# Kernel optimization log

Measured on AMD Instinct MI355X. Metric: run time of the kernel, lower is better.

## Reference

```python
import jax, jax.numpy as jnp
import numpy as np

CLIP = 1e5  # state-update clip bound from the original code

def _H(x):
    # smooth heaviside: (tanh(1e7*x)+1)/2
    return (jnp.tanh(1e7 * x) + 1.0) * 0.5

def _interception(Prec, PET, INSC):
    insc = jnp.clip(INSC * 5.0, 0.5, 5.0)
    IMAX = jnp.maximum(jnp.minimum(insc, PET), 0.0)
    INT = jnp.maximum(jnp.minimum(IMAX, Prec), 0.0)
    INR = jnp.maximum(Prec - INT, 0.0)
    return INT, INR

def _sms_store(SMS1, SMSC):
    S = jnp.clip(SMSC * 500.0, 50.0, 500.0)
    return jnp.maximum(jnp.minimum(SMS1, S), 0.0)

def _soil_fluxes(PET, INT, INR, COEFF, SQ, SMSC, SUB, CRAK, SMS1):
    C = jnp.clip(COEFF * 400.0, 50.0, 400.0)
    q = jnp.clip(SQ * 6.0, 0.0, 6.0)
    S = jnp.clip(SMSC * 500.0, 50.0, 500.0)
    sub = jnp.clip(SUB, 0.0, 1.0)
    crak = jnp.clip(CRAK, 0.0, 1.0)
    infil = C * jnp.exp(-q * SMS1 / S)
    RMO = jnp.maximum(_H(infil - INR) * INR + _H(INR - infil) * infil, 0.0)
    IRUN = jnp.maximum(INR - RMO, 0.0)
    SRUN = jnp.maximum(sub * (SMS1 / S) * RMO, 0.0)
    REC = jnp.maximum(crak * (SMS1 / S) * (RMO - SRUN), 0.0)
    SMF = jnp.maximum(RMO - SRUN - REC, 0.0)
    POT = jnp.maximum(PET - INT, 0.0)
    cap = 10.0 * SMS1 / S
    ETS = jnp.maximum(_H(cap - POT) * POT + _H(POT - cap) * cap, 0.0)
    return RMO, IRUN, SRUN, REC, SMF, ETS

def _recharge(SMS1, SMSC, REC, SMF, ETS):
    S = jnp.clip(SMSC * 500.0, 50.0, 500.0)
    x = SMS1 + SMF - ETS - S
    return jnp.maximum(_H(x) * (REC + x) + _H(-x) * REC, 0.0)

def _gw_store(GW1, RecK, LG):
    lg = jnp.clip(LG * 0.1, 0.001, 0.1)
    rk = jnp.clip(RecK * 0.3, 0.003, 0.3)
    BAS = jnp.maximum(_H(GW1) * (rk * GW1), 0.0)
    GWL1 = GW1 - lg
    return BAS, GWL1

def _release(RS, SRUN, IRUN, BAS, RSmax, Area, Kr):
    kr = jnp.clip(Kr * 0.1, 0.01, 0.1)
    inflow = (IRUN + SRUN + BAS) * Area
    x = RS + inflow - RSmax
    Q_or = jnp.maximum(_H(x) * x, 0.0)
    Q_ir = jnp.maximum(_H(x) * (kr * RSmax) + _H(-x) * kr * RS * jnp.power(RS / RSmax, 1.5), 0.0)
    Q_res_in = jnp.maximum(inflow, 0.0)
    return Q_res_in, Q_or, Q_ir

def setup_inputs():
    key = jax.random.key(0)
    B, T = 4096, 2048
    u = jax.random.uniform(key, (B, T, 4), dtype=jnp.float32)
    Prec = u[..., 0:1] * 20.0          # precipitation (mm/day)
    PET = u[..., 1:2] * 5.0            # potential ET
    RSmax = u[..., 2:3] * 100.0 + 10.0 # reservoir capacity (>0 to avoid div-by-0)
    Area = u[..., 3:4] * 0.5           # area ratio in (0, 0.5)
    inputs = jnp.concatenate([Prec, PET, RSmax, Area], axis=-1)
    p = lambda: jnp.full((1,), 0.5, jnp.float32)
    return dict(inputs=inputs, INSC=p(), COEFF=p(), SQ=p(), SMSC=p(), SUB=p(),
                CRAK=p(), RecK=p(), Kr=p(), LG=p(), LS=p())

def reference(inputs, INSC, COEFF, SQ, SMSC, SUB, CRAK, RecK, Kr, LG, LS):
    B, T, _ = inputs.shape
    x_t = jnp.transpose(inputs, (1, 0, 2))  # [T,B,4]

    def step(state, x):
        SMS1, GW1, RS = state[:, 0:1], state[:, 1:2], state[:, 2:3]
        Prec, PET, RSmax, Area = x[:, 0:1], x[:, 1:2], x[:, 2:3], x[:, 3:4]
        INT, INR = _interception(Prec, PET, INSC)
        SMS1c = _sms_store(SMS1, SMSC)
        _, IRUN, SRUN, REC, SMF, ETS = _soil_fluxes(PET, INT, INR, COEFF, SQ, SMSC, SUB, CRAK, SMS1c)
        next_SMS = SMS1c + jnp.clip(SMF - ETS, -CLIP, CLIP)
        RECnew = _recharge(SMS1c, SMSC, REC, SMF, ETS)
        BAS, GWL1 = _gw_store(GW1, RecK, LG)
        next_GW = GWL1 + jnp.clip(RECnew - BAS, -CLIP, CLIP)
        Q_res_in, Q_or, Q_ir = _release(RS, SRUN, IRUN, BAS, RSmax, Area, Kr)
        next_RS = RS + jnp.clip(Q_res_in - Q_or - Q_ir, -CLIP, CLIP)
        new = jnp.concatenate([next_SMS, next_GW, next_RS], axis=1)
        return new, new

    init = jnp.zeros((B, 3), inputs.dtype)
    _, outs = jax.lax.scan(step, init, x_t)
    outs = jnp.transpose(outs, (1, 0, 2))  # [B,T,3]

    # shift stores by one step (as in original call(): tf.roll shift=1 axis=1)
    SMS1 = jnp.roll(outs[:, :, 0:1], 1, axis=1)
    GW1 = jnp.roll(outs[:, :, 1:2], 1, axis=1)
    RS = outs[:, :, 2:3]

    Prec, PET, RSmax, Area = inputs[..., 0:1], inputs[..., 1:2], inputs[..., 2:3], inputs[..., 3:4]
    INT, INR = _interception(Prec, PET, INSC)
    SMS1 = _sms_store(SMS1, SMSC)
    _, IRUN, SRUN, _, _, _ = _soil_fluxes(PET, INT, INR, COEFF, SQ, SMSC, SUB, CRAK, SMS1)
    BAS, _ = _gw_store(GW1, RecK, LG)
    _, Q_or, Q_ir = _release(RS, SRUN, IRUN, BAS, RSmax, Area, Kr)
    ls = jnp.clip(LS * 10.0, 0.01, 10.0)
    dr_arg = (SRUN + IRUN) * (1.0 - Area) + Q_ir + Q_or - ls
    DR = jnp.maximum(_H(dr_arg) * dr_arg, 0.0)
    GD = BAS * (1.0 - Area)
    Q = jnp.maximum(DR + GD, 0.0)  # [B,T,1] generated flow ('normal' mode)
    return Q
```

## Files before the change

### kernel.cpp

```cpp
#include <hip/hip_runtime.h>

#define T_LEN  2048
#define NCH    4096
#define CH     64
#define NCHUNK (T_LEN / CH)
#define WARM   256
#define UNR    8

__device__ __forceinline__ float clampf(float x, float lo, float hi) {
    return fminf(fmaxf(x, lo), hi);
}

struct Params {
    float insc, C, S, sub, crak, rk, kr, lg, ls, invS, eca;
};

__device__ __forceinline__ Params mkparams(
    const float* pINSC, const float* pCOEFF, const float* pSQ, const float* pSMSC,
    const float* pSUB, const float* pCRAK, const float* pRecK, const float* pKr,
    const float* pLG, const float* pLS)
{
    Params pr;
    pr.insc = clampf(pINSC[0] * 5.f,   0.5f,   5.f);
    pr.C    = clampf(pCOEFF[0] * 400.f, 50.f,  400.f);
    float q = clampf(pSQ[0] * 6.f,     0.f,    6.f);
    pr.S    = clampf(pSMSC[0] * 500.f, 50.f,   500.f);
    pr.sub  = clampf(pSUB[0],          0.f,    1.f);
    pr.crak = clampf(pCRAK[0],         0.f,    1.f);
    pr.rk   = clampf(pRecK[0] * 0.3f,  0.003f, 0.3f);
    pr.kr   = clampf(pKr[0] * 0.1f,    0.01f,  0.1f);
    pr.lg   = clampf(pLG[0] * 0.1f,    0.001f, 0.1f);
    pr.ls   = clampf(pLS[0] * 10.f,    0.01f,  10.f);
    pr.invS = 1.0f / pr.S;
    pr.eca  = -q * pr.invS;
    return pr;
}

__global__ __launch_bounds__(256, 2)
void hirnn_chunk_kernel(const float* __restrict__ inp,
                        const float* __restrict__ pINSC, const float* __restrict__ pCOEFF,
                        const float* __restrict__ pSQ,   const float* __restrict__ pSMSC,
                        const float* __restrict__ pSUB,  const float* __restrict__ pCRAK,
                        const float* __restrict__ pRecK, const float* __restrict__ pKr,
                        const float* __restrict__ pLG,   const float* __restrict__ pLS,
                        float* __restrict__ out, float* __restrict__ ws)
{
    const int tid   = blockIdx.x * blockDim.x + threadIdx.x;
    const int chain = tid & (NCH - 1);
    const int chunk = tid >> 12;

    const Params pr = mkparams(pINSC, pCOEFF, pSQ, pSMSC, pSUB, pCRAK, pRecK, pKr, pLG, pLS);

    const float4* __restrict__ xin  = reinterpret_cast<const float4*>(inp) + (size_t)chain * T_LEN;
    float4* __restrict__       qout = reinterpret_cast<float4*>(out + (size_t)chain * T_LEN);

    const int t_start = chunk * CH;
    const int t_warm  = (t_start >= WARM) ? (t_start - WARM) : 0;
    const int t_end   = t_start + CH;

    float sms = 0.f, gw = 0.f, rs = 0.f;

    float4 bufA[UNR], bufB[UNR];
#pragma unroll
    for (int u = 0; u < UNR; ++u) bufA[u] = xin[t_warm + u];

    auto process = [&](const float4* buf, int t0) {
        float qstage[UNR];
#pragma unroll
        for (int u = 0; u < UNR; ++u) {
            const float p = buf[u].x, pet = buf[u].y, rsmax = buf[u].z, area = buf[u].w;

            const float INT  = fminf(fminf(pr.insc, pet), p);
            const float INR  = p - INT;
            const float smsc  = fminf(fmaxf(sms, 0.f), pr.S);
            const float ratio = smsc * pr.invS;
            const float infil = pr.C * __expf(pr.eca * smsc);
            const float RMO   = fminf(infil, INR);
            const float IRUN  = INR - RMO;
            const float SRUN  = pr.sub * ratio * RMO;
            const float REC   = pr.crak * ratio * (RMO - SRUN);
            const float SMF   = (RMO - SRUN) - REC;
            const float POT   = fmaxf(pet - INT, 0.f);
            const float ETS   = fminf(POT, 10.f * ratio);
            const float nsms  = smsc + (SMF - ETS);
            const float RECn  = REC + fmaxf(nsms - pr.S, 0.f);
            const float BAS   = pr.rk * fmaxf(gw, 0.f);
            const float ngw   = (gw - pr.lg) + (RECn - BAS);
            const float inflow = (IRUN + SRUN + BAS) * area;
            const float rinv   = __builtin_amdgcn_rcpf(rsmax);
            const float xr     = (rs + inflow) - rsmax;
            const float Qor    = fmaxf(xr, 0.f);
            const float rrt    = rs * rinv;
            const float Qir    = (xr > 0.f) ? (pr.kr * rsmax)
                                            : (pr.kr * rs * (rrt * __builtin_amdgcn_sqrtf(rrt)));
            const float nrs    = rs + ((inflow - Qor) - Qir);

            const float xq   = (nrs + inflow) - rsmax;
            const float Qor2 = fmaxf(xq, 0.f);
            const float r2   = nrs * rinv;
            const float Qir2 = (xq > 0.f) ? (pr.kr * rsmax)
                                          : (pr.kr * nrs * (r2 * __builtin_amdgcn_sqrtf(r2)));
            const float oma  = 1.f - area;
            const float dra  = (SRUN + IRUN) * oma + Qir2 + Qor2 - pr.ls;
            qstage[u] = fmaxf(fmaxf(dra, 0.f) + BAS * oma, 0.f);

            sms = nsms; gw = ngw; rs = nrs;
        }
        if (t0 >= t_start) {
#pragma unroll
            for (int v = 0; v < UNR / 4; ++v) {
                float4 w;
                w.x = qstage[4*v + 0]; w.y = qstage[4*v + 1];
                w.z = qstage[4*v + 2]; w.w = qstage[4*v + 3];
                qout[t0 / 4 + v] = w;
            }
        }
    };

    for (int t0 = t_warm; t0 < t_end; t0 += 2 * UNR) {
#pragma unroll
        for (int u = 0; u < UNR; ++u) bufB[u] = xin[t0 + UNR + u];
        process(bufA, t0);
        if (t0 + 2 * UNR < t_end) {
#pragma unroll
            for (int u = 0; u < UNR; ++u) bufA[u] = xin[t0 + 2 * UNR + u];
        }
        process(bufB, t0 + UNR);
    }

    if (chunk == NCHUNK - 1) {
        ws[chain * 2 + 0] = sms;
        ws[chain * 2 + 1] = gw;
    }
}

__global__ __launch_bounds__(256)
void hirnn_t0_kernel(const float* __restrict__ inp,
                     const float* __restrict__ pINSC, const float* __restrict__ pCOEFF,
                     const float* __restrict__ pSQ,   const float* __restrict__ pSMSC,
                     const float* __restrict__ pSUB,  const float* __restrict__ pCRAK,
                     const float* __restrict__ pRecK, const float* __restrict__ pKr,
                     const float* __restrict__ pLG,   const float* __restrict__ pLS,
                     const float* __restrict__ ws, float* __restrict__ out)
{
    const int b = blockIdx.x * blockDim.x + threadIdx.x;
    if (b >= NCH) return;

    const Params pr = mkparams(pINSC, pCOEFF, pSQ, pSMSC, pSUB, pCRAK, pRecK, pKr, pLG, pLS);

    const float4 x0 = reinterpret_cast<const float4*>(inp)[(size_t)b * T_LEN];
    const float p = x0.x, pet = x0.y, rsmax = x0.z, area = x0.w;

    const float INT = fminf(fminf(pr.insc, pet), p);
    const float INR = p - INT;

    const float RMO0   = fminf(pr.C, INR);
    const float IRUN0  = INR - RMO0;
    const float infl0  = IRUN0 * area;
    const float xr0    = infl0 - rsmax;
    const float Qor0   = fmaxf(xr0, 0.f);
    const float Qir0   = (xr0 > 0.f) ? (pr.kr * rsmax) : 0.f;
    const float rs0    = infl0 - Qor0 - Qir0;

    const float smsF  = ws[b * 2 + 0];
    const float gwF   = ws[b * 2 + 1];
    const float smsc  = fminf(fmaxf(smsF, 0.f), pr.S);
    const float ratio = smsc * pr.invS;
    const float infil = pr.C * __expf(pr.eca * smsc);
    const float RMO   = fminf(infil, INR);
    const float IRUN  = INR - RMO;
    const float SRUN  = pr.sub * ratio * RMO;
    const float BAS   = pr.rk * fmaxf(gwF, 0.f);

    const float inflow = (IRUN + SRUN + BAS) * area;
    const float rinv   = __builtin_amdgcn_rcpf(rsmax);
    const float xq     = (rs0 + inflow) - rsmax;
    const float Qor2   = fmaxf(xq, 0.f);
    const float r2     = rs0 * rinv;
    const float Qir2   = (xq > 0.f) ? (pr.kr * rsmax)
                                    : (pr.kr * rs0 * (r2 * __builtin_amdgcn_sqrtf(r2)));
    const float oma    = 1.f - area;
    const float dra    = (SRUN + IRUN) * oma + Qir2 + Qor2 - pr.ls;
    out[(size_t)b * T_LEN] = fmaxf(fmaxf(dra, 0.f) + BAS * oma, 0.f);
}

extern "C" void kernel_launch(void* const* d_in, const int* in_sizes, int n_in,
                              void* d_out, int out_size, void* d_ws, size_t ws_size,
                              hipStream_t stream) {
    const float* inp = (const float*)d_in[0];
    float* out = (float*)d_out;
    float* ws  = (float*)d_ws;

    const int threads = NCH * NCHUNK;
    hirnn_chunk_kernel<<<threads / 256, 256, 0, stream>>>(
        inp,
        (const float*)d_in[1], (const float*)d_in[2], (const float*)d_in[3],
        (const float*)d_in[4], (const float*)d_in[5], (const float*)d_in[6],
        (const float*)d_in[7], (const float*)d_in[8], (const float*)d_in[9],
        (const float*)d_in[10],
        out, ws);

    hirnn_t0_kernel<<<NCH / 256, 256, 0, stream>>>(
        inp,
        (const float*)d_in[1], (const float*)d_in[2], (const float*)d_in[3],
        (const float*)d_in[4], (const float*)d_in[5], (const float*)d_in[6],
        (const float*)d_in[7], (const float*)d_in[8], (const float*)d_in[9],
        (const float*)d_in[10],
        ws, out);
}
```

Before: 310.0 us.

## Deepen input prefetch to four buffers and skip output math during warmup

Replaces the double-buffered input prefetch with a four-deep rotating register buffer, so loads are issued further ahead of the serial recurrence. Splits the time loop into a warmup phase that runs a template step without the output (second reservoir evaluation) computation, and an output phase that computes and stores flows. It also drops a redundant max on POT, which is nonnegative by construction. More live float4 registers may raise register pressure and lower occupancy.

```diff
diff --git a/kernel.cpp b/kernel.cpp
--- a/kernel.cpp
+++ b/kernel.cpp
@@ -6,6 +6,7 @@
 #define NCHUNK (T_LEN / CH)
 #define WARM   256
 #define UNR    8
+#define NBUF   4
 
 __device__ __forceinline__ float clampf(float x, float lo, float hi) {
     return fminf(fmaxf(x, lo), hi);
@@ -36,6 +37,53 @@
     return pr;
 }
 
+template <bool OUT>
+__device__ __forceinline__ float step_one(const Params& pr, const float4& xv,
+                                          float& sms, float& gw, float& rs)
+{
+    const float p = xv.x, pet = xv.y, rsmax = xv.z, area = xv.w;
+
+    const float INT  = fminf(fminf(pr.insc, pet), p);
+    const float INR  = p - INT;
+    const float smsc  = fminf(fmaxf(sms, 0.f), pr.S);
+    const float ratio = smsc * pr.invS;
+    const float infil = pr.C * __expf(pr.eca * smsc);
+    const float RMO   = fminf(infil, INR);
+    const float IRUN  = INR - RMO;
+    const float SRUN  = pr.sub * ratio * RMO;
+    const float REC   = pr.crak * ratio * (RMO - SRUN);
+    const float SMF   = (RMO - SRUN) - REC;
+    const float POT   = pet - INT;
+    const float ETS   = fminf(POT, 10.f * ratio);
+    const float nsms  = smsc + (SMF - ETS);
+    const float RECn  = REC + fmaxf(nsms - pr.S, 0.f);
+    const float BAS   = pr.rk * fmaxf(gw, 0.f);
+    const float ngw   = (gw - pr.lg) + (RECn - BAS);
+    const float inflow = (IRUN + SRUN + BAS) * area;
+    const float rinv   = __builtin_amdgcn_rcpf(rsmax);
+    const float xr     = (rs + inflow) - rsmax;
+    const float Qor    = fmaxf(xr, 0.f);
+    const float rrt    = rs * rinv;
+    const float Qir    = (xr > 0.f) ? (pr.kr * rsmax)
+                                    : (pr.kr * rs * (rrt * __builtin_amdgcn_sqrtf(rrt)));
+    const float nrs    = rs + ((inflow - Qor) - Qir);
+
+    float q = 0.f;
+    if constexpr (OUT) {
+        const float xq   = (nrs + inflow) - rsmax;
+        const float Qor2 = fmaxf(xq, 0.f);
+        const float r2   = nrs * rinv;
+        const float Qir2 = (xq > 0.f) ? (pr.kr * rsmax)
+                                      : (pr.kr * nrs * (r2 * __builtin_amdgcn_sqrtf(r2)));
+        const float oma  = 1.f - area;
+        const float dra  = (SRUN + IRUN) * oma + Qir2 + Qor2 - pr.ls;
+        q = fmaxf(fmaxf(dra, 0.f) + BAS * oma, 0.f);
+    }
+
+    sms = nsms; gw = ngw; rs = nrs;
+    return q;
+}
+
 __global__ __launch_bounds__(256, 2)
 void hirnn_chunk_kernel(const float* __restrict__ inp,
                         const float* __restrict__ pINSC, const float* __restrict__ pCOEFF,
@@ -60,72 +108,92 @@
 
     float sms = 0.f, gw = 0.f, rs = 0.f;
 
-    float4 bufA[UNR], bufB[UNR];
-#pragma unroll
-    for (int u = 0; u < UNR; ++u) bufA[u] = xin[t_warm + u];
-
-    auto process = [&](const float4* buf, int t0) {
-        float qstage[UNR];
-#pragma unroll
-        for (int u = 0; u < UNR; ++u) {
-            const float p = buf[u].x, pet = buf[u].y, rsmax = buf[u].z, area = buf[u].w;
-
-            const float INT  = fminf(fminf(pr.insc, pet), p);
-            const float INR  = p - INT;
-            const float smsc  = fminf(fmaxf(sms, 0.f), pr.S);
-            const float ratio = smsc * pr.invS;
-            const float infil = pr.C * __expf(pr.eca * smsc);
-            const float RMO   = fminf(infil, INR);
-            const float IRUN  = INR - RMO;
-            const float SRUN  = pr.sub * ratio * RMO;
-            const float REC   = pr.crak * ratio * (RMO - SRUN);
-            const float SMF   = (RMO - SRUN) - REC;
-            const float POT   = fmaxf(pet - INT, 0.f);
-            const float ETS   = fminf(POT, 10.f * ratio);
-            const float nsms  = smsc + (SMF - ETS);
-            const float RECn  = REC + fmaxf(nsms - pr.S, 0.f);
-            const float BAS   = pr.rk * fmaxf(gw, 0.f);
-            const float ngw   = (gw - pr.lg) + (RECn - BAS);
-            const float inflow = (IRUN + SRUN + BAS) * area;
-            const float rinv   = __builtin_amdgcn_rcpf(rsmax);
-            const float xr     = (rs + inflow) - rsmax;
-            const float Qor    = fmaxf(xr, 0.f);
-            const float rrt    = rs * rinv;
-            const float Qir    = (xr > 0.f) ? (pr.kr * rsmax)
-                                            : (pr.kr * rs * (rrt * __builtin_amdgcn_sqrtf(rrt)));
-            const float nrs    = rs + ((inflow - Qor) - Qir);
-
-            const float xq   = (nrs + inflow) - rsmax;
-            const float Qor2 = fmaxf(xq, 0.f);
-            const float r2   = nrs * rinv;
-            const float Qir2 = (xq > 0.f) ? (pr.kr * rsmax)
-                                          : (pr.kr * nrs * (r2 * __builtin_amdgcn_sqrtf(r2)));
-            const float oma  = 1.f - area;
-            const float dra  = (SRUN + IRUN) * oma + Qir2 + Qor2 - pr.ls;
-            qstage[u] = fmaxf(fmaxf(dra, 0.f) + BAS * oma, 0.f);
-
-            sms = nsms; gw = ngw; rs = nrs;
-        }
-        if (t0 >= t_start) {
-#pragma unroll
-            for (int v = 0; v < UNR / 4; ++v) {
-                float4 w;
-                w.x = qstage[4*v + 0]; w.y = qstage[4*v + 1];
-                w.z = qstage[4*v + 2]; w.w = qstage[4*v + 3];
-                qout[t0 / 4 + v] = w;
-            }
-        }
-    };
-
-    for (int t0 = t_warm; t0 < t_end; t0 += 2 * UNR) {
-#pragma unroll
-        for (int u = 0; u < UNR; ++u) bufB[u] = xin[t0 + UNR + u];
-        process(bufA, t0);
-        if (t0 + 2 * UNR < t_end) {
-#pragma unroll
-            for (int u = 0; u < UNR; ++u) bufA[u] = xin[t0 + 2 * UNR + u];
-        }
-        process(bufB, t0 + UNR);
+    float4 b0[UNR], b1[UNR], b2[UNR], b3[UNR];
+#pragma unroll
+    for (int u = 0; u < UNR; ++u) {
+        b0[u] = xin[t_warm + 0 * UNR + u];
+        b1[u] = xin[t_warm + 1 * UNR + u];
+        b2[u] = xin[t_warm + 2 * UNR + u];
+        b3[u] = xin[t_warm + 3 * UNR + u];
+    }
+
+    for (int t0 = t_warm; t0 < t_start; t0 += NBUF * UNR) {
+#pragma unroll
+        for (int u = 0; u < UNR; ++u) step_one<false>(pr, b0[u], sms, gw, rs);
+#pragma unroll
+        for (int u = 0; u < UNR; ++u) b0[u] = xin[t0 + 4 * UNR + u];
+#pragma unroll
+        for (int u = 0; u < UNR; ++u) step_one<false>(pr, b1[u], sms, gw, rs);
+#pragma unroll
+        for (int u = 0; u < UNR; ++u) b1[u] = xin[t0 + 5 * UNR + u];
+#pragma unroll
+        for (int u = 0; u < UNR; ++u) step_one<false>(pr, b2[u], sms, gw, rs);
+#pragma unroll
+        for (int u = 0; u < UNR; ++u) b2[u] = xin[t0 + 6 * UNR + u];
+#pragma unroll
+        for (int u = 0; u < UNR; ++u) step_one<false>(pr, b3[u], sms, gw, rs);
+#pragma unroll
+        for (int u = 0; u < UNR; ++u) b3[u] = xin[t0 + 7 * UNR + u];
+    }
+
+    for (int t0 = t_start; t0 < t_end; t0 += NBUF * UNR) {
+        float q[UNR];
+
+#pragma unroll
+        for (int u = 0; u < UNR; ++u) q[u] = step_one<true>(pr, b0[u], sms, gw, rs);
+        {
+            float4 w0, w1;
+            w0.x = q[0]; w0.y = q[1]; w0.z = q[2]; w0.w = q[3];
+            w1.x = q[4]; w1.y = q[5]; w1.z = q[6]; w1.w = q[7];
+            qout[(t0 + 0 * UNR) / 4 + 0] = w0;
+            qout[(t0 + 0 * UNR) / 4 + 1] = w1;
+        }
+        if (t0 + 4 * UNR < t_end) {
+#pragma unroll
+            for (int u = 0; u < UNR; ++u) b0[u] = xin[t0 + 4 * UNR + u];
+        }
+
+#pragma unroll
+        for (int u = 0; u < UNR; ++u) q[u] = step_one<true>(pr, b1[u], sms, gw, rs);
+        {
+            float4 w0, w1;
+            w0.x = q[0]; w0.y = q[1]; w0.z = q[2]; w0.w = q[3];
+            w1.x = q[4]; w1.y = q[5]; w1.z = q[6]; w1.w = q[7];
+            qout[(t0 + 1 * UNR) / 4 + 0] = w0;
+            qout[(t0 + 1 * UNR) / 4 + 1] = w1;
+        }
+        if (t0 + 5 * UNR < t_end) {
+#pragma unroll
+            for (int u = 0; u < UNR; ++u) b1[u] = xin[t0 + 5 * UNR + u];
+        }
+
+#pragma unroll
+        for (int u = 0; u < UNR; ++u) q[u] = step_one<true>(pr, b2[u], sms, gw, rs);
+        {
+            float4 w0, w1;
+            w0.x = q[0]; w0.y = q[1]; w0.z = q[2]; w0.w = q[3];
+            w1.x = q[4]; w1.y = q[5]; w1.z = q[6]; w1.w = q[7];
+            qout[(t0 + 2 * UNR) / 4 + 0] = w0;
+            qout[(t0 + 2 * UNR) / 4 + 1] = w1;
+        }
+        if (t0 + 6 * UNR < t_end) {
+#pragma unroll
+            for (int u = 0; u < UNR; ++u) b2[u] = xin[t0 + 6 * UNR + u];
+        }
+
+#pragma unroll
+        for (int u = 0; u < UNR; ++u) q[u] = step_one<true>(pr, b3[u], sms, gw, rs);
+        {
+            float4 w0, w1;
+            w0.x = q[0]; w0.y = q[1]; w0.z = q[2]; w0.w = q[3];
+            w1.x = q[4]; w1.y = q[5]; w1.z = q[6]; w1.w = q[7];
+            qout[(t0 + 3 * UNR) / 4 + 0] = w0;
+            qout[(t0 + 3 * UNR) / 4 + 1] = w1;
+        }
+        if (t0 + 7 * UNR < t_end) {
+#pragma unroll
+            for (int u = 0; u < UNR; ++u) b3[u] = xin[t0 + 7 * UNR + u];
+        }
     }
 
     if (chunk == NCHUNK - 1) {
```

Measured after the change: 298.4 us. -3.7%, faster.

## Stage input through swizzled LDS for coalesced loads and skip output math during warmup

Applied to the files above, without the earlier changes.

Input loads now go through shared memory. Groups of 8 threads read 8 consecutive timesteps of one chain with coalesced float4 loads and write them into an XOR-swizzled, double-buffered LDS tile. Each thread then reads its own chain's timesteps back from LDS. The old pattern had each thread stride through its own row, and this change targets that poor coalescing. A templated step function also skips the output-flow computation during warmup steps, and POT's max with zero is dropped because pet >= INT always holds. The cost is a __syncthreads per 8 timesteps and 32KB of LDS per block, which may limit occupancy.

```diff
diff --git a/kernel.cpp b/kernel.cpp
--- a/kernel.cpp
+++ b/kernel.cpp
@@ -5,7 +5,8 @@
 #define CH     64
 #define NCHUNK (T_LEN / CH)
 #define WARM   256
-#define UNR    8
+#define CPB    256
+#define TK     8
 
 __device__ __forceinline__ float clampf(float x, float lo, float hi) {
     return fminf(fmaxf(x, lo), hi);
@@ -36,6 +37,53 @@
     return pr;
 }
 
+template <bool OUT>
+__device__ __forceinline__ float step_one(const Params& pr, const float4& xv,
+                                          float& sms, float& gw, float& rs)
+{
+    const float p = xv.x, pet = xv.y, rsmax = xv.z, area = xv.w;
+
+    const float INT  = fminf(fminf(pr.insc, pet), p);
+    const float INR  = p - INT;
+    const float smsc  = fminf(fmaxf(sms, 0.f), pr.S);
+    const float ratio = smsc * pr.invS;
+    const float infil = pr.C * __expf(pr.eca * smsc);
+    const float RMO   = fminf(infil, INR);
+    const float IRUN  = INR - RMO;
+    const float SRUN  = pr.sub * ratio * RMO;
+    const float REC   = pr.crak * ratio * (RMO - SRUN);
+    const float SMF   = (RMO - SRUN) - REC;
+    const float POT   = pet - INT;
+    const float ETS   = fminf(POT, 10.f * ratio);
+    const float nsms  = smsc + (SMF - ETS);
+    const float RECn  = REC + fmaxf(nsms - pr.S, 0.f);
+    const float BAS   = pr.rk * fmaxf(gw, 0.f);
+    const float ngw   = (gw - pr.lg) + (RECn - BAS);
+    const float inflow = (IRUN + SRUN + BAS) * area;
+    const float rinv   = __builtin_amdgcn_rcpf(rsmax);
+    const float xr     = (rs + inflow) - rsmax;
+    const float Qor    = fmaxf(xr, 0.f);
+    const float rrt    = rs * rinv;
+    const float Qir    = (xr > 0.f) ? (pr.kr * rsmax)
+                                    : (pr.kr * rs * (rrt * __builtin_amdgcn_sqrtf(rrt)));
+    const float nrs    = rs + ((inflow - Qor) - Qir);
+
+    float q = 0.f;
+    if constexpr (OUT) {
+        const float xq   = (nrs + inflow) - rsmax;
+        const float Qor2 = fmaxf(xq, 0.f);
+        const float r2   = nrs * rinv;
+        const float Qir2 = (xq > 0.f) ? (pr.kr * rsmax)
+                                      : (pr.kr * nrs * (r2 * __builtin_amdgcn_sqrtf(r2)));
+        const float oma  = 1.f - area;
+        const float dra  = (SRUN + IRUN) * oma + Qir2 + Qor2 - pr.ls;
+        q = fmaxf(fmaxf(dra, 0.f) + BAS * oma, 0.f);
+    }
+
+    sms = nsms; gw = ngw; rs = nrs;
+    return q;
+}
+
 __global__ __launch_bounds__(256, 2)
 void hirnn_chunk_kernel(const float* __restrict__ inp,
                         const float* __restrict__ pINSC, const float* __restrict__ pCOEFF,
@@ -45,14 +93,25 @@
                         const float* __restrict__ pLG,   const float* __restrict__ pLS,
                         float* __restrict__ out, float* __restrict__ ws)
 {
-    const int tid   = blockIdx.x * blockDim.x + threadIdx.x;
-    const int chain = tid & (NCH - 1);
-    const int chunk = tid >> 12;
+    __shared__ float4 lds[2][CPB * TK];
+
+    const int tid   = threadIdx.x;
+    const int blk   = blockIdx.x;
+    const int chunk = blk >> 4;
+    const int cgrp  = blk & 15;
+    const int chain = cgrp * CPB + tid;
 
     const Params pr = mkparams(pINSC, pCOEFF, pSQ, pSMSC, pSUB, pCRAK, pRecK, pKr, pLG, pLS);
 
-    const float4* __restrict__ xin  = reinterpret_cast<const float4*>(inp) + (size_t)chain * T_LEN;
-    float4* __restrict__       qout = reinterpret_cast<float4*>(out + (size_t)chain * T_LEN);
+    const int sIdx = tid & 7;
+    const int gRow = tid >> 3;
+    const float4* __restrict__ gbase =
+        reinterpret_cast<const float4*>(inp) + (size_t)(cgrp * CPB) * T_LEN;
+    const int stBase = gRow * TK + (sIdx ^ (gRow & 7));
+    const int rdBase = tid * TK;
+    const int rdX    = tid & 7;
+
+    float4* __restrict__ qout = reinterpret_cast<float4*>(out + (size_t)chain * T_LEN);
 
     const int t_start = chunk * CH;
     const int t_warm  = (t_start >= WARM) ? (t_start - WARM) : 0;
@@ -60,72 +119,43 @@
 
     float sms = 0.f, gw = 0.f, rs = 0.f;
 
-    float4 bufA[UNR], bufB[UNR];
-#pragma unroll
-    for (int u = 0; u < UNR; ++u) bufA[u] = xin[t_warm + u];
-
-    auto process = [&](const float4* buf, int t0) {
-        float qstage[UNR];
-#pragma unroll
-        for (int u = 0; u < UNR; ++u) {
-            const float p = buf[u].x, pet = buf[u].y, rsmax = buf[u].z, area = buf[u].w;
-
-            const float INT  = fminf(fminf(pr.insc, pet), p);
-            const float INR  = p - INT;
-            const float smsc  = fminf(fmaxf(sms, 0.f), pr.S);
-            const float ratio = smsc * pr.invS;
-            const float infil = pr.C * __expf(pr.eca * smsc);
-            const float RMO   = fminf(infil, INR);
-            const float IRUN  = INR - RMO;
-            const float SRUN  = pr.sub * ratio * RMO;
-            const float REC   = pr.crak * ratio * (RMO - SRUN);
-            const float SMF   = (RMO - SRUN) - REC;
-            const float POT   = fmaxf(pet - INT, 0.f);
-            const float ETS   = fminf(POT, 10.f * ratio);
-            const float nsms  = smsc + (SMF - ETS);
-            const float RECn  = REC + fmaxf(nsms - pr.S, 0.f);
-            const float BAS   = pr.rk * fmaxf(gw, 0.f);
-            const float ngw   = (gw - pr.lg) + (RECn - BAS);
-            const float inflow = (IRUN + SRUN + BAS) * area;
-            const float rinv   = __builtin_amdgcn_rcpf(rsmax);
-            const float xr     = (rs + inflow) - rsmax;
-            const float Qor    = fmaxf(xr, 0.f);
-            const float rrt    = rs * rinv;
-            const float Qir    = (xr > 0.f) ? (pr.kr * rsmax)
-                                            : (pr.kr * rs * (rrt * __builtin_amdgcn_sqrtf(rrt)));
-            const float nrs    = rs + ((inflow - Qor) - Qir);
-
-            const float xq   = (nrs + inflow) - rsmax;
-            const float Qor2 = fmaxf(xq, 0.f);
-            const float r2   = nrs * rinv;
-            const float Qir2 = (xq > 0.f) ? (pr.kr * rsmax)
-                                          : (pr.kr * nrs * (r2 * __builtin_amdgcn_sqrtf(r2)));
-            const float oma  = 1.f - area;
-            const float dra  = (SRUN + IRUN) * oma + Qir2 + Qor2 - pr.ls;
-            qstage[u] = fmaxf(fmaxf(dra, 0.f) + BAS * oma, 0.f);
-
-            sms = nsms; gw = ngw; rs = nrs;
+    float4 r[TK];
+#pragma unroll
+    for (int k = 0; k < TK; ++k)
+        r[k] = gbase[(size_t)(k * 32 + gRow) * T_LEN + t_warm + sIdx];
+
+    int p = 0;
+    for (int t0 = t_warm; t0 < t_end; t0 += TK, p ^= 1) {
+#pragma unroll
+        for (int k = 0; k < TK; ++k)
+            lds[p][stBase + k * 32 * TK] = r[k];
+
+        if (t0 + TK < t_end) {
+#pragma unroll
+            for (int k = 0; k < TK; ++k)
+                r[k] = gbase[(size_t)(k * 32 + gRow) * T_LEN + (t0 + TK) + sIdx];
         }
-        if (t0 >= t_start) {
-#pragma unroll
-            for (int v = 0; v < UNR / 4; ++v) {
-                float4 w;
-                w.x = qstage[4*v + 0]; w.y = qstage[4*v + 1];
-                w.z = qstage[4*v + 2]; w.w = qstage[4*v + 3];
-                qout[t0 / 4 + v] = w;
-            }
+
+        __syncthreads();
+
+        float4 x[TK];
+#pragma unroll
+        for (int s = 0; s < TK; ++s)
+            x[s] = lds[p][rdBase + (s ^ rdX)];
+
+        if (t0 < t_start) {
+#pragma unroll
+            for (int s = 0; s < TK; ++s) step_one<false>(pr, x[s], sms, gw, rs);
+        } else {
+            float q[TK];
+#pragma unroll
+            for (int s = 0; s < TK; ++s) q[s] = step_one<true>(pr, x[s], sms, gw, rs);
+            float4 w0, w1;
+            w0.x = q[0]; w0.y = q[1]; w0.z = q[2]; w0.w = q[3];
+            w1.x = q[4]; w1.y = q[5]; w1.z = q[6]; w1.w = q[7];
+            qout[t0 / 4 + 0] = w0;
+            qout[t0 / 4 + 1] = w1;
         }
-    };
-
-    for (int t0 = t_warm; t0 < t_end; t0 += 2 * UNR) {
-#pragma unroll
-        for (int u = 0; u < UNR; ++u) bufB[u] = xin[t0 + UNR + u];
-        process(bufA, t0);
-        if (t0 + 2 * UNR < t_end) {
-#pragma unroll
-            for (int u = 0; u < UNR; ++u) bufA[u] = xin[t0 + 2 * UNR + u];
-        }
-        process(bufB, t0 + UNR);
     }
 
     if (chunk == NCHUNK - 1) {
@@ -191,8 +221,8 @@
     float* out = (float*)d_out;
     float* ws  = (float*)d_ws;
 
-    const int threads = NCH * NCHUNK;
-    hirnn_chunk_kernel<<<threads / 256, 256, 0, stream>>>(
+    const int blocks = (NCH / CPB) * NCHUNK;
+    hirnn_chunk_kernel<<<blocks, CPB, 0, stream>>>(
         inp,
         (const float*)d_in[1], (const float*)d_in[2], (const float*)d_in[3],
         (const float*)d_in[4], (const float*)d_in[5], (const float*)d_in[6],
```

Result: slower. 460.1 us (+48.4%).
